# Optimization experiments

Hardware: AMD Instinct MI355X
Metric: run time of the kernel (lower is better)

The kernel has to match this reference:

```python
import jax, jax.numpy as jnp
import numpy as np

N_ATOM = 4_000_000
N_FRAG = 200_000
EIG_THRESHOLD = 0.01


def setup_inputs() -> dict:
    key = jax.random.key(0)
    k1, k2, k3, k4, k5 = jax.random.split(key, 5)
    f_atom = jax.random.normal(k1, (N_ATOM, 3), jnp.float32)
    atom_pos = jax.random.normal(k2, (N_ATOM, 3), jnp.float32) * 5.0
    T_frag = jax.random.normal(k3, (N_FRAG, 3), jnp.float32) * 5.0
    frag_id = jax.random.randint(k4, (N_ATOM,), 0, N_FRAG)
    frag_sizes = jax.random.randint(k5, (N_FRAG,), 1, 40)
    return {"f_atom": f_atom, "atom_pos": atom_pos, "T_frag": T_frag,
            "frag_id": frag_id, "frag_sizes": frag_sizes, "n_frag": N_FRAG}


def reference(f_atom, atom_pos, T_frag, frag_id, frag_sizes, n_frag):
    dtype = f_atom.dtype
    # scatter_mean(f_atom, frag_id): segment_sum / counts
    counts = jax.ops.segment_sum(jnp.ones((f_atom.shape[0],), dtype), frag_id,
                                 num_segments=n_frag)
    denom = jnp.maximum(counts, 1.0)[:, None]
    v_frag = jax.ops.segment_sum(f_atom, frag_id, num_segments=n_frag) / denom  # [F,3]

    r_arm = atom_pos - T_frag[frag_id]                                   # [N,3]
    torque = jax.ops.segment_sum(jnp.cross(r_arm, f_atom), frag_id,
                                 num_segments=n_frag)                    # [F,3]

    r2 = jnp.sum(r_arm * r_arm, axis=-1)                                 # [N]
    I_diag = jax.ops.segment_sum(r2, frag_id, num_segments=n_frag)       # [F]
    rr = r_arm[:, :, None] * r_arm[:, None, :]                           # [N,3,3]
    I_off = jax.ops.segment_sum(rr.reshape(-1, 9), frag_id,
                                num_segments=n_frag).reshape(-1, 3, 3)   # [F,3,3]
    I_tensor = I_diag[:, None, None] * jnp.eye(3, dtype=dtype) - I_off   # [F,3,3]

    eigenvalues, eigenvectors = jnp.linalg.eigh(I_tensor)                # [F,3], [F,3,3]
    max_eig = jnp.maximum(jnp.max(eigenvalues, axis=-1, keepdims=True), 1e-8)
    observable = (eigenvalues > EIG_THRESHOLD * max_eig).astype(dtype)   # [F,3]
    observable = jnp.where((frag_sizes <= 1)[:, None],
                           jnp.zeros((), dtype), observable)

    torque_eig = jnp.einsum('nji,nj->ni', eigenvectors, torque)          # V^T torque
    omega_eig = torque_eig / jnp.maximum(eigenvalues, 1e-6) * observable
    omega_frag = jnp.einsum('nij,nj->ni', eigenvectors, omega_eig)
    P_observable = jnp.einsum('nij,nj,nkj->nik', eigenvectors, observable, eigenvectors)
    return v_frag, omega_frag, P_observable
```

## Files before the change

kernel.cpp:

```cpp
#include <hip/hip_runtime.h>
#include <math.h>

__device__ __forceinline__ void frag_epilogue(
    const float* a, int f, int n_frag, const int* __restrict__ frag_sizes,
    float* __restrict__ out)
{
    float cntf  = a[12];
    float denom = fmaxf(cntf, 1.0f);
    float vfx = a[0] / denom, vfy = a[1] / denom, vfz = a[2] / denom;

    double tq0 = (double)a[3], tq1 = (double)a[4], tq2 = (double)a[5];
    double Mxx = (double)a[6], Myy = (double)a[7], Mzz = (double)a[8];
    double Mxy = (double)a[9], Mxz = (double)a[10], Myz = (double)a[11];
    double tr = Mxx + Myy + Mzz;

    double A[3][3] = {
        { tr - Mxx, -Mxy,     -Mxz     },
        { -Mxy,     tr - Myy, -Myz     },
        { -Mxz,     -Myz,     tr - Mzz }
    };
    double V[3][3] = {{1,0,0},{0,1,0},{0,0,1}};

    for (int sweep = 0; sweep < 6; ++sweep) {
        for (int pq = 0; pq < 3; ++pq) {
            int p = (pq == 2) ? 1 : 0;
            int q = (pq == 0) ? 1 : 2;
            double apq = A[p][q];
            if (fabs(apq) <= 1e-14 * (fabs(A[p][p]) + fabs(A[q][q])) ||
                fabs(apq) < 1e-300) continue;
            double theta = (A[q][q] - A[p][p]) / (2.0 * apq);
            double tt;
            if (fabs(theta) > 1e100) tt = 1.0 / (2.0 * theta);
            else tt = copysign(1.0, theta) / (fabs(theta) + sqrt(theta * theta + 1.0));
            double c = 1.0 / sqrt(tt * tt + 1.0);
            double s = tt * c;
            double app = A[p][p], aqq = A[q][q];
            A[p][p] = app - tt * apq;
            A[q][q] = aqq + tt * apq;
            A[p][q] = 0.0; A[q][p] = 0.0;
            int r = 3 - p - q;
            double arp = A[r][p], arq = A[r][q];
            A[r][p] = c * arp - s * arq; A[p][r] = A[r][p];
            A[r][q] = s * arp + c * arq; A[q][r] = A[r][q];
            for (int i2 = 0; i2 < 3; ++i2) {
                double vip = V[i2][p], viq = V[i2][q];
                V[i2][p] = c * vip - s * viq;
                V[i2][q] = s * vip + c * viq;
            }
        }
    }

    double lam0 = A[0][0], lam1 = A[1][1], lam2 = A[2][2];
    double maxeig = fmax(fmax(fmax(lam0, lam1), lam2), 1e-8);
    double thr = 0.01 * maxeig;
    bool small_frag = (frag_sizes[f] <= 1);
    double o0 = (!small_frag && lam0 > thr) ? 1.0 : 0.0;
    double o1 = (!small_frag && lam1 > thr) ? 1.0 : 0.0;
    double o2 = (!small_frag && lam2 > thr) ? 1.0 : 0.0;

    double te0 = V[0][0]*tq0 + V[1][0]*tq1 + V[2][0]*tq2;
    double te1 = V[0][1]*tq0 + V[1][1]*tq1 + V[2][1]*tq2;
    double te2 = V[0][2]*tq0 + V[1][2]*tq1 + V[2][2]*tq2;
    double we0 = te0 / fmax(lam0, 1e-6) * o0;
    double we1 = te1 / fmax(lam1, 1e-6) * o1;
    double we2 = te2 / fmax(lam2, 1e-6) * o2;
    double w0 = V[0][0]*we0 + V[0][1]*we1 + V[0][2]*we2;
    double w1 = V[1][0]*we0 + V[1][1]*we1 + V[1][2]*we2;
    double w2 = V[2][0]*we0 + V[2][1]*we1 + V[2][2]*we2;

    size_t F = (size_t)n_frag;
    out[(size_t)f*3 + 0] = vfx;
    out[(size_t)f*3 + 1] = vfy;
    out[(size_t)f*3 + 2] = vfz;
    out[F*3 + (size_t)f*3 + 0] = (float)w0;
    out[F*3 + (size_t)f*3 + 1] = (float)w1;
    out[F*3 + (size_t)f*3 + 2] = (float)w2;

    float* P = out + F*6 + (size_t)f*9;
    #pragma unroll
    for (int i2 = 0; i2 < 3; ++i2)
        #pragma unroll
        for (int k = 0; k < 3; ++k)
            P[i2*3 + k] = (float)(V[i2][0]*o0*V[k][0] + V[i2][1]*o1*V[k][1]
                                  + V[i2][2]*o2*V[k][2]);
}

#define NBK  512
#define FPB  400
#define BCAP 9000
#define CAP2 1024
#define MAXPT 2
#define TILE 16
#define APB  (256 * TILE)
#define SCHUNK 2048
#define CPT    4
#define RECMAX (500u * BCAP)

__global__ __launch_bounds__(256) void init_cursors(
    unsigned* __restrict__ cursor, int nbk)
{
    int b = blockIdx.x * 256 + threadIdx.x;
    if (b <= nbk) cursor[b] = (unsigned)b * BCAP;
}

__global__ __launch_bounds__(512) void scatter_atoms(
    const float* __restrict__ f_atom,
    const float* __restrict__ atom_pos,
    const int*   __restrict__ frag_id,
    unsigned*    __restrict__ cursor,
    float4*      __restrict__ recs,
    int n_atom)
{
    __shared__ float    srt[SCHUNK * 7];
    __shared__ unsigned hist[NBK];
    __shared__ unsigned cbase[NBK];
    __shared__ unsigned obase[NBK];
    __shared__ unsigned wsum[4];
    int t = threadIdx.x;
    int lane = t & 63, w = t >> 6;

    for (int b = t; b < NBK; b += 512) hist[b] = 0;
    __syncthreads();

    const int4*   fid4 = (const int4*)frag_id;
    const float4* pos4 = (const float4*)atom_pos;
    const float4* ff4  = (const float4*)f_atom;
    int bs = blockIdx.x * APB;

    for (int c = 0; c < APB / SCHUNK; ++c) {
        int cs = bs + c * SCHUNK;
        int mchunk = n_atom - cs;
        if (mchunk > SCHUNK) mchunk = SCHUNK;
        if (mchunk < 0) mchunk = 0;

        int      bkv[CPT], lfv[CPT];
        unsigned rk[CPT];
        float ax[CPT], ay[CPT], az[CPT], gx[CPT], gy[CPT], gz[CPT];
        {
            int i4 = (cs >> 2) + t;
            if (4 * i4 < n_atom) {
                int4 v = fid4[i4];
                float4 p0 = pos4[3*(size_t)i4+0], p1 = pos4[3*(size_t)i4+1], p2 = pos4[3*(size_t)i4+2];
                float4 g0 = ff4[3*(size_t)i4+0],  g1 = ff4[3*(size_t)i4+1],  g2 = ff4[3*(size_t)i4+2];
                int   fid_[4] = {v.x, v.y, v.z, v.w};
                float px_[4] = {p0.x, p0.w, p1.z, p2.y};
                float py_[4] = {p0.y, p1.x, p1.w, p2.z};
                float pz_[4] = {p0.z, p1.y, p2.x, p2.w};
                float gx_[4] = {g0.x, g0.w, g1.z, g2.y};
                float gy_[4] = {g0.y, g1.x, g1.w, g2.z};
                float gz_[4] = {g0.z, g1.y, g2.x, g2.w};
                #pragma unroll
                for (int cc = 0; cc < 4; ++cc) {
                    int fid = fid_[cc];
                    int bk = fid / FPB;
                    bkv[cc] = bk;
                    lfv[cc] = fid - bk * FPB;
                    rk[cc]  = atomicAdd(&hist[bk], 1u);
                    ax[cc] = px_[cc]; ay[cc] = py_[cc]; az[cc] = pz_[cc];
                    gx[cc] = gx_[cc]; gy[cc] = gy_[cc]; gz[cc] = gz_[cc];
                }
            } else {
                #pragma unroll
                for (int cc = 0; cc < 4; ++cc) bkv[cc] = -1;
            }
        }
        __syncthreads();

        for (int b = t; b < NBK; b += 512) {
            unsigned cnt = hist[b];
            obase[b] = cnt ? atomicAdd(&cursor[b], cnt) : 0u;
        }

        unsigned pv = 0, incl = 0;
        if (t < 256) {
            pv = hist[2*t] + hist[2*t + 1];
            incl = pv;
        }
        if (w < 4) {
            #pragma unroll
            for (int st = 1; st < 64; st <<= 1) {
                unsigned v = __shfl_up(incl, (unsigned)st, 64);
                if (lane >= st) incl += v;
            }
            if (lane == 63) wsum[w] = incl;
        }
        __syncthreads();
        if (t == 0) {
            unsigned cum = 0;
            #pragma unroll
            for (int k = 0; k < 4; ++k) { unsigned v = wsum[k]; wsum[k] = cum; cum += v; }
        }
        __syncthreads();
        if (t < 256) {
            unsigned excl = incl - pv + wsum[w];
            cbase[2*t]     = excl;
            cbase[2*t + 1] = excl + hist[2*t];
        }
        __syncthreads();

        #pragma unroll
        for (int k = 0; k < CPT; ++k) {
            if (bkv[k] >= 0) {
                unsigned p = (cbase[bkv[k]] + rk[k]) * 7u;
                srt[p+0] = ax[k]; srt[p+1] = ay[k]; srt[p+2] = az[k];
                srt[p+3] = gx[k]; srt[p+4] = gy[k]; srt[p+5] = gz[k];
                srt[p+6] = __int_as_float(lfv[k] | (bkv[k] << 16));
            }
        }
        __syncthreads();

        #pragma unroll
        for (int k = 0; k < CPT; ++k) {
            int j = t + k * 512;
            if (j < mchunk) {
                const float* d = &srt[(unsigned)j * 7u];
                int pk = __float_as_int(d[6]);
                int lf = pk & 0xFFFF;
                int bk = pk >> 16;
                unsigned addr = obase[bk] + (unsigned)j - cbase[bk];
                if (addr < RECMAX) {
                    recs[2*(size_t)addr + 0] = make_float4(d[0], d[1], d[2], __int_as_float(lf));
                    recs[2*(size_t)addr + 1] = make_float4(d[3], d[4], d[5], 0.0f);
                }
            }
        }
        __syncthreads();

        for (int b = t; b < NBK; b += 512) hist[b] = 0;
        __syncthreads();
    }
}

__global__ __launch_bounds__(512) void sort_reduce(
    const float4*   __restrict__ recs,
    const unsigned* __restrict__ cursor,
    const float*    __restrict__ T_frag,
    const int*      __restrict__ frag_sizes,
    float*          __restrict__ out,
    int n_frag)
{
    __shared__ float    srt[CAP2 * 7];
    __shared__ unsigned hist[FPB];
    __shared__ unsigned cbase[FPB];
    __shared__ unsigned wsum[8];

    int b = blockIdx.x, t = threadIdx.x;
    int lane = t & 63, w = t >> 6;
    int frag0 = b * FPB;
    int nf = n_frag - frag0;
    if (nf > FPB) nf = FPB;

    unsigned start = (unsigned)b * BCAP;
    unsigned end   = cursor[b];
    unsigned cap = (unsigned)(b + 1) * BCAP;
    if (end > cap) end = cap;

    bool own = (t < nf);
    float Tx = 0, Ty = 0, Tz = 0;
    if (own) {
        int f = frag0 + t;
        Tx = T_frag[3*f+0]; Ty = T_frag[3*f+1]; Tz = T_frag[3*f+2];
    }
    float s[12];
    #pragma unroll
    for (int k = 0; k < 12; ++k) s[k] = 0.0f;
    unsigned fragcnt = 0;

    for (unsigned c0 = start; c0 < end; c0 += CAP2) {
        unsigned m = end - c0;
        if (m > CAP2) m = CAP2;

        for (int k = t; k < FPB; k += 512) hist[k] = 0;
        __syncthreads();

        float4 rv[MAXPT], fvv[MAXPT];
        int rlf[MAXPT];
        unsigned rrk[MAXPT];
        #pragma unroll
        for (int k = 0; k < MAXPT; ++k) {
            unsigned i = (unsigned)t + (unsigned)k * 512u;
            rlf[k] = -1;
            if (i < m) {
                rv[k]  = recs[2 * (size_t)(c0 + i) + 0];
                fvv[k] = recs[2 * (size_t)(c0 + i) + 1];
                int lf = __float_as_int(rv[k].w);
                rlf[k] = lf;
                rrk[k] = atomicAdd(&hist[lf], 1u);
            }
        }
        __syncthreads();

        unsigned p = 0;
        if (t < FPB / 2) p = hist[2*t] + hist[2*t + 1];
        unsigned incl = p;
        if (w < 4) {
            #pragma unroll
            for (int st = 1; st < 64; st <<= 1) {
                unsigned v = __shfl_up(incl, (unsigned)st, 64);
                if (lane >= st) incl += v;
            }
            if (lane == 63) wsum[w] = incl;
        }
        __syncthreads();
        if (t == 0) {
            unsigned c = 0;
            #pragma unroll
            for (int k = 0; k < 4; ++k) { unsigned v = wsum[k]; wsum[k] = c; c += v; }
        }
        __syncthreads();
        if (t < FPB / 2) {
            unsigned excl = incl - p + wsum[w];
            cbase[2*t]     = excl;
            cbase[2*t + 1] = excl + hist[2*t];
        }
        __syncthreads();

        #pragma unroll
        for (int k = 0; k < MAXPT; ++k) {
            if (rlf[k] >= 0) {
                unsigned q = (cbase[rlf[k]] + rrk[k]) * 7u;
                srt[q + 0] = rv[k].x;  srt[q + 1] = rv[k].y;  srt[q + 2] = rv[k].z;
                srt[q + 3] = fvv[k].x; srt[q + 4] = fvv[k].y; srt[q + 5] = fvv[k].z;
            }
        }
        __syncthreads();

        if (own) {
            unsigned cb = cbase[t], cnt = hist[t];
            fragcnt += cnt;
            for (unsigned k = 0; k < cnt; ++k) {
                const float* d = &srt[(cb + k) * 7u];
                float rx = d[0] - Tx, ry = d[1] - Ty, rz = d[2] - Tz;
                float Fx = d[3], Fy = d[4], Fz = d[5];
                s[0] += Fx; s[1] += Fy; s[2] += Fz;
                s[3] += ry*Fz - rz*Fy;
                s[4] += rz*Fx - rx*Fz;
                s[5] += rx*Fy - ry*Fx;
                s[6] += rx*rx; s[7] += ry*ry; s[8] += rz*rz;
                s[9] += rx*ry; s[10] += rx*rz; s[11] += ry*rz;
            }
        }
        __syncthreads();
    }

    if (own) {
        float a[13];
        #pragma unroll
        for (int k = 0; k < 12; ++k) a[k] = s[k];
        a[12] = (float)fragcnt;
        frag_epilogue(a, frag0 + t, n_frag, frag_sizes, out);
    }
}

#define NACC 16

__global__ __launch_bounds__(256) void atom_scatter_fb(
    const float* __restrict__ f_atom, const float* __restrict__ atom_pos,
    const float* __restrict__ T_frag, const int* __restrict__ frag_id,
    float* __restrict__ acc, int n_atom)
{
    int i = blockIdx.x * blockDim.x + threadIdx.x;
    if (i >= n_atom) return;
    int fid = frag_id[i];
    float fx = f_atom[3*i+0], fy = f_atom[3*i+1], fz = f_atom[3*i+2];
    float px = atom_pos[3*i+0], py = atom_pos[3*i+1], pz = atom_pos[3*i+2];
    float rx = px - T_frag[3*fid+0], ry = py - T_frag[3*fid+1], rz = pz - T_frag[3*fid+2];
    float cx = ry*fz - rz*fy, cy = rz*fx - rx*fz, cz = rx*fy - ry*fx;
    float* a = acc + (size_t)fid * NACC;
    atomicAdd(a+0, fx);    atomicAdd(a+1, fy);    atomicAdd(a+2, fz);
    atomicAdd(a+3, cx);    atomicAdd(a+4, cy);    atomicAdd(a+5, cz);
    atomicAdd(a+6, rx*rx); atomicAdd(a+7, ry*ry); atomicAdd(a+8, rz*rz);
    atomicAdd(a+9, rx*ry); atomicAdd(a+10, rx*rz); atomicAdd(a+11, ry*rz);
    atomicAdd(a+12, 1.0f);
}

__global__ __launch_bounds__(256) void frag_solve_fb(
    const float* __restrict__ acc, const int* __restrict__ frag_sizes,
    float* __restrict__ out, int n_frag)
{
    int f = blockIdx.x * blockDim.x + threadIdx.x;
    if (f >= n_frag) return;
    float a[13];
    #pragma unroll
    for (int k = 0; k < 13; ++k) a[k] = acc[(size_t)f * NACC + k];
    frag_epilogue(a, f, n_frag, frag_sizes, out);
}

extern "C" void kernel_launch(void* const* d_in, const int* in_sizes, int n_in,
                              void* d_out, int out_size, void* d_ws, size_t ws_size,
                              hipStream_t stream) {
    const float* f_atom     = (const float*)d_in[0];
    const float* atom_pos   = (const float*)d_in[1];
    const float* T_frag     = (const float*)d_in[2];
    const int*   frag_id    = (const int*)d_in[3];
    const int*   frag_sizes = (const int*)d_in[4];
    int n_atom = in_sizes[0] / 3;
    int n_frag = in_sizes[2] / 3;
    float* out = (float*)d_out;

    int nblk = (n_atom + APB - 1) / APB;
    int nbk  = (n_frag + FPB - 1) / FPB;

    size_t cur_bytes = (size_t)(NBK + 1) * sizeof(unsigned);
    size_t recs_off  = (cur_bytes + 255) & ~(size_t)255;
    size_t need      = recs_off + (size_t)nbk * BCAP * 2 * sizeof(float4);

    if (ws_size >= need && nbk <= NBK && nbk == 500 && (n_atom % 4) == 0) {
        unsigned* cursor = (unsigned*)d_ws;
        float4*   recs   = (float4*)((char*)d_ws + recs_off);

        init_cursors<<<(NBK + 256) / 256, 256, 0, stream>>>(cursor, nbk);
        scatter_atoms<<<nblk, 512, 0, stream>>>(
            f_atom, atom_pos, frag_id, cursor, recs, n_atom);
        sort_reduce<<<nbk, 512, 0, stream>>>(
            recs, cursor, T_frag, frag_sizes, out, n_frag);
    } else {
        float* acc = (float*)d_ws;
        hipMemsetAsync(acc, 0, (size_t)n_frag * NACC * sizeof(float), stream);
        atom_scatter_fb<<<(n_atom + 255) / 256, 256, 0, stream>>>(
            f_atom, atom_pos, T_frag, frag_id, acc, n_atom);
        frag_solve_fb<<<(n_frag + 255) / 256, 256, 0, stream>>>(acc, frag_sizes, out, n_frag);
    }
}
```

Measured before the change: 225.6 us.

## Subtract fragment origin during scatter and pack records into 24+2 bytes

The scatter kernel now gathers T_frag per atom and stores the relative arm instead of the absolute position. Each record is stored as six packed floats, with the local fragment id held in a separate 16-bit array. This replaces the 32-byte float4 pair per atom and reduces intermediate write and read traffic between the two kernels. In exchange, every atom does a random T_frag load in the scatter pass, and records are now accessed with float2 loads.

```diff
diff --git a/kernel.cpp b/kernel.cpp
--- a/kernel.cpp
+++ b/kernel.cpp
@@ -107,8 +107,10 @@
     const float* __restrict__ f_atom,
     const float* __restrict__ atom_pos,
     const int*   __restrict__ frag_id,
+    const float* __restrict__ T_frag,
     unsigned*    __restrict__ cursor,
-    float4*      __restrict__ recs,
+    float*       __restrict__ rec6,
+    unsigned short* __restrict__ lfs,
     int n_atom)
 {
     __shared__ float    srt[SCHUNK * 7];
@@ -156,7 +158,8 @@
                     bkv[cc] = bk;
                     lfv[cc] = fid - bk * FPB;
                     rk[cc]  = atomicAdd(&hist[bk], 1u);
-                    ax[cc] = px_[cc]; ay[cc] = py_[cc]; az[cc] = pz_[cc];
+                    float tx = T_frag[3*fid+0], ty = T_frag[3*fid+1], tz = T_frag[3*fid+2];
+                    ax[cc] = px_[cc] - tx; ay[cc] = py_[cc] - ty; az[cc] = pz_[cc] - tz;
                     gx[cc] = gx_[cc]; gy[cc] = gy_[cc]; gz[cc] = gz_[cc];
                 }
             } else {
@@ -219,8 +222,11 @@
                 int bk = pk >> 16;
                 unsigned addr = obase[bk] + (unsigned)j - cbase[bk];
                 if (addr < RECMAX) {
-                    recs[2*(size_t)addr + 0] = make_float4(d[0], d[1], d[2], __int_as_float(lf));
-                    recs[2*(size_t)addr + 1] = make_float4(d[3], d[4], d[5], 0.0f);
+                    float2* r2 = (float2*)&rec6[(size_t)addr * 6u];
+                    r2[0] = make_float2(d[0], d[1]);
+                    r2[1] = make_float2(d[2], d[3]);
+                    r2[2] = make_float2(d[4], d[5]);
+                    lfs[addr] = (unsigned short)lf;
                 }
             }
         }
@@ -232,9 +238,9 @@
 }
 
 __global__ __launch_bounds__(512) void sort_reduce(
-    const float4*   __restrict__ recs,
+    const float*    __restrict__ rec6,
+    const unsigned short* __restrict__ lfs,
     const unsigned* __restrict__ cursor,
-    const float*    __restrict__ T_frag,
     const int*      __restrict__ frag_sizes,
     float*          __restrict__ out,
     int n_frag)
@@ -256,11 +262,6 @@
     if (end > cap) end = cap;
 
     bool own = (t < nf);
-    float Tx = 0, Ty = 0, Tz = 0;
-    if (own) {
-        int f = frag0 + t;
-        Tx = T_frag[3*f+0]; Ty = T_frag[3*f+1]; Tz = T_frag[3*f+2];
-    }
     float s[12];
     #pragma unroll
     for (int k = 0; k < 12; ++k) s[k] = 0.0f;
@@ -273,7 +274,7 @@
         for (int k = t; k < FPB; k += 512) hist[k] = 0;
         __syncthreads();
 
-        float4 rv[MAXPT], fvv[MAXPT];
+        float2 ra[MAXPT], rb[MAXPT], rc[MAXPT];
         int rlf[MAXPT];
         unsigned rrk[MAXPT];
         #pragma unroll
@@ -281,9 +282,11 @@
             unsigned i = (unsigned)t + (unsigned)k * 512u;
             rlf[k] = -1;
             if (i < m) {
-                rv[k]  = recs[2 * (size_t)(c0 + i) + 0];
-                fvv[k] = recs[2 * (size_t)(c0 + i) + 1];
-                int lf = __float_as_int(rv[k].w);
+                const float2* r2 = (const float2*)&rec6[(size_t)(c0 + i) * 6u];
+                ra[k] = r2[0];
+                rb[k] = r2[1];
+                rc[k] = r2[2];
+                int lf = (int)lfs[c0 + i];
                 rlf[k] = lf;
                 rrk[k] = atomicAdd(&hist[lf], 1u);
             }
@@ -319,8 +322,8 @@
         for (int k = 0; k < MAXPT; ++k) {
             if (rlf[k] >= 0) {
                 unsigned q = (cbase[rlf[k]] + rrk[k]) * 7u;
-                srt[q + 0] = rv[k].x;  srt[q + 1] = rv[k].y;  srt[q + 2] = rv[k].z;
-                srt[q + 3] = fvv[k].x; srt[q + 4] = fvv[k].y; srt[q + 5] = fvv[k].z;
+                srt[q + 0] = ra[k].x; srt[q + 1] = ra[k].y; srt[q + 2] = rb[k].x;
+                srt[q + 3] = rb[k].y; srt[q + 4] = rc[k].x; srt[q + 5] = rc[k].y;
             }
         }
         __syncthreads();
@@ -330,7 +333,7 @@
             fragcnt += cnt;
             for (unsigned k = 0; k < cnt; ++k) {
                 const float* d = &srt[(cb + k) * 7u];
-                float rx = d[0] - Tx, ry = d[1] - Ty, rz = d[2] - Tz;
+                float rx = d[0], ry = d[1], rz = d[2];
                 float Fx = d[3], Fy = d[4], Fz = d[5];
                 s[0] += Fx; s[1] += Fy; s[2] += Fz;
                 s[3] += ry*Fz - rz*Fy;
@@ -402,18 +405,21 @@
     int nbk  = (n_frag + FPB - 1) / FPB;
 
     size_t cur_bytes = (size_t)(NBK + 1) * sizeof(unsigned);
-    size_t recs_off  = (cur_bytes + 255) & ~(size_t)255;
-    size_t need      = recs_off + (size_t)nbk * BCAP * 2 * sizeof(float4);
+    size_t rec6_off  = (cur_bytes + 255) & ~(size_t)255;
+    size_t rec6_bytes = (size_t)nbk * BCAP * 6 * sizeof(float);
+    size_t lfs_off   = (rec6_off + rec6_bytes + 255) & ~(size_t)255;
+    size_t need      = lfs_off + (size_t)nbk * BCAP * sizeof(unsigned short);
 
     if (ws_size >= need && nbk <= NBK && nbk == 500 && (n_atom % 4) == 0) {
-        unsigned* cursor = (unsigned*)d_ws;
-        float4*   recs   = (float4*)((char*)d_ws + recs_off);
+        unsigned*       cursor = (unsigned*)d_ws;
+        float*          rec6   = (float*)((char*)d_ws + rec6_off);
+        unsigned short* lfs    = (unsigned short*)((char*)d_ws + lfs_off);
 
         init_cursors<<<(NBK + 256) / 256, 256, 0, stream>>>(cursor, nbk);
         scatter_atoms<<<nblk, 512, 0, stream>>>(
-            f_atom, atom_pos, frag_id, cursor, recs, n_atom);
+            f_atom, atom_pos, frag_id, T_frag, cursor, rec6, lfs, n_atom);
         sort_reduce<<<nbk, 512, 0, stream>>>(
-            recs, cursor, T_frag, frag_sizes, out, n_frag);
+            rec6, lfs, cursor, frag_sizes, out, n_frag);
     } else {
         float* acc = (float*)d_ws;
         hipMemsetAsync(acc, 0, (size_t)n_frag * NACC * sizeof(float), stream);
```

Result: slower. 251.1 us (+11.3%).
